# Kernel optimization log

Measured on AMD Instinct MI355X. Metric: run time of the kernel, lower is better.

The kernel has to match this reference:

```python
import jax, jax.numpy as jnp
import numpy as np

N_NODES = 50000
N_EDGES = 800000
D_IN = 128
D_OUT = 128
N_GRAPHS = 512
N_CONVS = 5
EPS = 1e-5


def setup_inputs() -> dict:
    key = jax.random.key(0)
    ks = jax.random.split(key, 8)
    x = jax.random.normal(ks[0], (N_NODES, D_IN), dtype=jnp.float32)
    edge_index = jax.random.randint(ks[1], (2, N_EDGES), 0, N_NODES, dtype=jnp.int32)
    batch = jnp.sort(jax.random.randint(ks[2], (N_NODES,), 0, N_GRAPHS, dtype=jnp.int32))
    s = 1.0 / np.sqrt(D_IN)
    W_rel = jax.random.normal(ks[3], (N_CONVS, D_OUT, D_IN), dtype=jnp.float32) * s
    b_rel = jax.random.normal(ks[4], (N_CONVS, D_OUT), dtype=jnp.float32) * s
    W_root = jax.random.normal(ks[5], (N_CONVS, D_OUT, D_IN), dtype=jnp.float32) * s
    gamma = jnp.ones((D_OUT,), dtype=jnp.float32)
    beta = jnp.zeros((D_OUT,), dtype=jnp.float32)
    Wc = jax.random.normal(ks[6], (96, D_OUT), dtype=jnp.float32) * (1.0 / np.sqrt(D_OUT))
    bc = jax.random.normal(ks[7], (96,), dtype=jnp.float32) * (1.0 / np.sqrt(D_OUT))
    return {"x": x, "edge_index": edge_index, "batch": batch, "i": 0,
            "W_rel": W_rel, "b_rel": b_rel, "W_root": W_root,
            "gamma": gamma, "beta": beta, "Wc": Wc, "bc": bc}


def reference(x, edge_index, batch, i, W_rel, b_rel, W_root, gamma, beta, Wc, bc):
    # --- 5 GraphConv branches, summed. GraphConv: lin_rel(sum_{j->i} x_j) + lin_root(x).
    # Sum over the 5 convs commutes with the linears, so fold the weights first.
    src, dst = edge_index[0], edge_index[1]
    agg = jax.ops.segment_sum(x[src], dst, num_segments=N_NODES)  # [N, D_in]
    Wr = jnp.sum(W_rel, axis=0)   # [D_out, D_in]
    Wt = jnp.sum(W_root, axis=0)  # [D_out, D_in]
    br = jnp.sum(b_rel, axis=0)   # [D_out]
    h = agg @ Wr.T + x @ Wt.T + br  # [N, D_out]
    # --- NodeLevelBatchNorm (training: batch stats over all nodes, biased var)
    mean = jnp.mean(h, axis=0)
    var = jnp.mean((h - mean) ** 2, axis=0)
    h = gamma * (h - mean) * jax.lax.rsqrt(var + EPS) + beta
    # --- global max pool over graphs, relu, classifier (i=0 -> no-dropout branch)
    pooled = jax.ops.segment_max(h, batch, num_segments=N_GRAPHS)  # [G, D_out]
    pooled = jax.nn.relu(pooled)
    return pooled @ Wc.T + bc  # [G, 96]
```

## Files before the change

### kernel.cpp

```cpp
#include <hip/hip_runtime.h>

#define EPS 1e-5f

constexpr int NN = 50000, NE = 800000, DD = 128, NG = 512, NC = 5, NO = 96;
constexpr int MAXB = 8192;
constexpr int NBUCK = 196;

typedef __attribute__((ext_vector_type(8))) short bf16x8;
typedef __attribute__((ext_vector_type(4))) float f32x4;

constexpr size_t HB   = 0;
constexpr size_t XB   = (size_t)NN * DD / 2;
constexpr size_t WB   = XB + (size_t)NN * DD / 2;
constexpr size_t BRO  = WB + DD * 256 / 2;
constexpr size_t CSUM = BRO + DD;
constexpr size_t CSQ  = CSUM + DD;
constexpr size_t POOL = CSQ + DD;
constexpr size_t GCNT = POOL + (size_t)NG * DD;
constexpr size_t ZEND = GCNT + 256;
constexpr size_t ROFF = ZEND;
constexpr size_t BSTOR= ROFF + NN + 1;
constexpr size_t CSR16= BSTOR + (size_t)NBUCK*MAXB;

constexpr int XCAST_B = NN * DD / 4 / 256;
constexpr int FOLD_B  = DD * DD / 256;
constexpr int BUCK_B  = (NE + 4095) / 4096;

static __device__ __forceinline__ unsigned short f2b(float f) {
    unsigned int u = __float_as_uint(f);
    return (unsigned short)((u + 0x7FFFu + ((u >> 16) & 1u)) >> 16);
}
static __device__ __forceinline__ float b2f(unsigned short h) {
    return __uint_as_float(((unsigned int)h) << 16);
}
static __device__ __forceinline__ unsigned fkey(float f) {
    unsigned u = __float_as_uint(f);
    return (u >> 31) ? ~u : (u | 0x80000000u);
}
static __device__ __forceinline__ float unfkey(unsigned k) {
    unsigned u = (k & 0x80000000u) ? (k ^ 0x80000000u) : ~k;
    return __uint_as_float(u);
}

__global__ __launch_bounds__(256) void k_prep(const float* __restrict__ x,
                                              const float* __restrict__ Wrel,
                                              const float* __restrict__ brel,
                                              const float* __restrict__ Wroot,
                                              const int* __restrict__ ei,
                                              float* __restrict__ ws, int* __restrict__ wi) {
    __shared__ int lcnt[256];
    __shared__ int lbase[256];
    int b = blockIdx.x, t = threadIdx.x;
    if (b < XCAST_B) {
        int i = b * 256 + t;
        float4 v = ((const float4*)x)[i];
        ushort4 o = {f2b(v.x), f2b(v.y), f2b(v.z), f2b(v.w)};
        ((ushort4*)(ws + XB))[i] = o;
    } else if (b < XCAST_B + FOLD_B) {
        int idx = (b - XCAST_B) * 256 + t;
        int k = idx >> 7, o = idx & 127;
        float wr = 0.f, wt = 0.f;
        for (int c = 0; c < NC; ++c) {
            wr += Wrel [c*DD*DD + o*DD + k];
            wt += Wroot[c*DD*DD + o*DD + k];
        }
        unsigned short* wb = (unsigned short*)(ws + WB);
        wb[o*256 + k]       = f2b(wr);
        wb[o*256 + 128 + k] = f2b(wt);
        if (k == 0) {
            float bias = 0.f;
            for (int c = 0; c < NC; ++c) bias += brel[c*DD + o];
            ws[BRO + o] = bias;
        }
    } else {
        int bb = b - XCAST_B - FOLD_B;
        lcnt[t] = 0;
        __syncthreads();
        int val[16], krk[16];
        #pragma unroll
        for (int j = 0; j < 16; ++j) {
            int e = bb * 4096 + j * 256 + t;
            krk[j] = -1;
            if (e < NE) {
                int d = ei[NE + e], s = ei[e];
                int key = d >> 8;
                int r = atomicAdd(&lcnt[key], 1);
                val[j] = s | ((d & 255) << 16);
                krk[j] = (key << 16) | r;
            }
        }
        __syncthreads();
        if (t < NBUCK && lcnt[t] > 0)
            lbase[t] = atomicAdd(&wi[GCNT + t], lcnt[t]);
        __syncthreads();
        #pragma unroll
        for (int j = 0; j < 16; ++j) {
            if (krk[j] >= 0) {
                int key = krk[j] >> 16, r = krk[j] & 0xFFFF;
                int p = lbase[key] + r;
                if (p < MAXB) wi[BSTOR + (size_t)key * MAXB + p] = val[j];
            }
        }
    }
}

__global__ __launch_bounds__(256) void k_sort(int* __restrict__ wi) {
    __shared__ int eds[MAXB];
    __shared__ unsigned short srt[MAXB];
    __shared__ int cnt[256], cnt2[256], lscan[256], gall[256];
    int t = threadIdx.x, b = blockIdx.x;
    int g = wi[GCNT + t];
    gall[t] = g; lscan[t] = g; cnt[t] = 0;
    __syncthreads();
    for (int off = 1; off < 256; off <<= 1) {
        int u = (t >= off) ? gall[t - off] : 0;
        __syncthreads();
        gall[t] += u;
        __syncthreads();
    }
    int base = gall[b] - lscan[b];
    int C = lscan[b]; if (C > MAXB) C = MAXB;
    __syncthreads();
    for (int i = t; i < C; i += 256) {
        int v = wi[BSTOR + (size_t)b * MAXB + i];
        eds[i] = v;
        atomicAdd(&cnt[v >> 16], 1);
    }
    __syncthreads();
    int cv = cnt[t];
    for (int off = 1; off < 256; off <<= 1) {
        int u = (t >= off) ? cnt[t - off] : 0;
        __syncthreads();
        cnt[t] += u;
        __syncthreads();
    }
    lscan[t] = cnt[t] - cv;
    cnt2[t] = 0;
    __syncthreads();
    int n = b * 256 + t;
    if (n < NN) wi[ROFF + n] = base + lscan[t];
    if (b == 0 && t == 0) wi[ROFF + NN] = NE;
    for (int i = t; i < C; i += 256) {
        int v = eds[i], k = v >> 16;
        int p = lscan[k] + atomicAdd(&cnt2[k], 1);
        srt[p] = (unsigned short)(v & 0xFFFF);
    }
    __syncthreads();
    unsigned short* csr = (unsigned short*)(wi + CSR16);
    for (int i = t; i < C; i += 256)
        csr[base + i] = srt[i];
}

__global__ __launch_bounds__(256) void k_gather(const int* __restrict__ wi,
                                                float* __restrict__ ws) {
    const unsigned short* xb = (const unsigned short*)(ws + XB);
    const unsigned short* csr = (const unsigned short*)(wi + CSR16);
    unsigned short* hb = (unsigned short*)(ws + HB);
    int tid = threadIdx.x;
    int n   = blockIdx.x * 16 + (tid >> 4);
    int sub = tid & 15;
    int c8  = sub * 8;
    if (n >= NN) return;
    int e0 = wi[ROFF + n], e1 = wi[ROFF + n + 1];
    int cnt = e1 - e0;
    float acc0[8] = {}, acc1[8] = {};
    int base = 0;
    for (; base + 16 <= cnt; base += 16) {
        int myE = (int)csr[e0 + base + sub];
        #pragma unroll
        for (int h = 0; h < 2; ++h) {
            bf16x8 v[8];
            #pragma unroll
            for (int j = 0; j < 8; ++j) {
                int s = __shfl(myE, h * 8 + j, 16);
                v[j] = *(const bf16x8*)&xb[(size_t)s * DD + c8];
            }
            #pragma unroll
            for (int j = 0; j < 8; ++j)
                #pragma unroll
                for (int c = 0; c < 8; ++c)
                    ((j & 1) ? acc1 : acc0)[c] += b2f((unsigned short)v[j][c]);
        }
    }
    int rem = cnt - base;
    if (rem > 0) {
        int myE = (sub < rem) ? (int)csr[e0 + base + sub] : 0;
        int j = 0;
        for (; j + 8 <= rem; j += 8) {
            bf16x8 v[8];
            #pragma unroll
            for (int q = 0; q < 8; ++q) {
                int s = __shfl(myE, j + q, 16);
                v[q] = *(const bf16x8*)&xb[(size_t)s * DD + c8];
            }
            #pragma unroll
            for (int q = 0; q < 8; ++q)
                #pragma unroll
                for (int c = 0; c < 8; ++c)
                    ((q & 1) ? acc1 : acc0)[c] += b2f((unsigned short)v[q][c]);
        }
        if (j + 4 <= rem) {
            bf16x8 v[4];
            #pragma unroll
            for (int q = 0; q < 4; ++q) {
                int s = __shfl(myE, j + q, 16);
                v[q] = *(const bf16x8*)&xb[(size_t)s * DD + c8];
            }
            #pragma unroll
            for (int q = 0; q < 4; ++q)
                #pragma unroll
                for (int c = 0; c < 8; ++c)
                    ((q & 1) ? acc1 : acc0)[c] += b2f((unsigned short)v[q][c]);
            j += 4;
        }
        for (; j < rem; ++j) {
            int s = __shfl(myE, j, 16);
            bf16x8 v = *(const bf16x8*)&xb[(size_t)s * DD + c8];
            #pragma unroll
            for (int c = 0; c < 8; ++c) acc0[c] += b2f((unsigned short)v[c]);
        }
    }
    bf16x8 o;
    #pragma unroll
    for (int c = 0; c < 8; ++c) o[c] = (short)f2b(acc0[c] + acc1[c]);
    *(bf16x8*)&hb[(size_t)n * DD + c8] = o;
}

__global__ __launch_bounds__(256) void k_gemm(const int* __restrict__ batch,
                                              float* __restrict__ ws) {
    __shared__ float sSum[128], sSq[128];
    __shared__ int batchS[128];
    __shared__ unsigned maxS[32][128];
    const unsigned short* hb = (const unsigned short*)(ws + HB);
    const unsigned short* xb = (const unsigned short*)(ws + XB);
    const unsigned short* wb = (const unsigned short*)(ws + WB);
    unsigned* poolU = (unsigned*)(ws + POOL);
    int tid  = threadIdx.x;
    if (tid < 128) { sSum[tid] = 0.f; sSq[tid] = 0.f; }
    for (int i = tid; i < 32 * 128; i += 256) ((unsigned*)maxS)[i] = 0u;
    if (tid < 128) {
        int r = blockIdx.x * 128 + tid; if (r > NN - 1) r = NN - 1;
        batchS[tid] = batch[r];
    }
    __syncthreads();
    int gBase = batchS[0];
    int wave = tid >> 6, lane = tid & 63;
    int ch = wave & 1, rg = wave >> 1;
    int quad = lane >> 4, l16 = lane & 15;
    bf16x8 bf[4][8];
    #pragma unroll
    for (int nt = 0; nt < 4; ++nt)
        #pragma unroll
        for (int kt = 0; kt < 8; ++kt)
            bf[nt][kt] = *(const bf16x8*)(wb + (size_t)(ch*64 + nt*16 + l16)*256 + kt*32 + quad*8);
    float bias[4], csum[4] = {}, csq[4] = {};
    #pragma unroll
    for (int nt = 0; nt < 4; ++nt) bias[nt] = ws[BRO + ch*64 + nt*16 + l16];
    #pragma unroll
    for (int c = 0; c < 4; ++c) {
        int lbase = rg * 64 + c * 16;
        int row0 = blockIdx.x * 128 + lbase;
        int arow = row0 + l16; if (arow > NN - 1) arow = NN - 1;
        const unsigned short* aggRow = hb + (size_t)arow * DD;
        const unsigned short* xRow   = xb + (size_t)arow * DD;
        bf16x8 af[8];
        #pragma unroll
        for (int kt = 0; kt < 8; ++kt)
            af[kt] = *(const bf16x8*)((kt < 4 ? aggRow + kt*32 : xRow + kt*32 - 128) + quad*8);
        f32x4 acc[4] = {};
        #pragma unroll
        for (int kt = 0; kt < 8; ++kt)
            #pragma unroll
            for (int nt = 0; nt < 4; ++nt)
                acc[nt] = __builtin_amdgcn_mfma_f32_16x16x32_bf16(af[kt], bf[nt][kt], acc[nt], 0, 0, 0);
        #pragma unroll
        for (int nt = 0; nt < 4; ++nt) {
            int col = ch*64 + nt*16 + l16;
            float mx = 0.f; int gcur = -1;
            #pragma unroll
            for (int r = 0; r < 4; ++r) {
                int row = row0 + quad*4 + r;
                if (row < NN) {
                    float v = acc[nt][r] + bias[nt];
                    csum[nt] += v; csq[nt] += v * v;
                    int g = batchS[lbase + quad*4 + r];
                    if (g != gcur) {
                        if (gcur >= 0) {
                            int rel = gcur - gBase;
                            if (rel < 32) atomicMax(&maxS[rel][col], fkey(mx));
                            else atomicMax(&poolU[(size_t)gcur * DD + col], fkey(mx));
                        }
                        gcur = g; mx = v;
                    } else mx = fmaxf(mx, v);
                }
            }
            if (gcur >= 0) {
                int rel = gcur - gBase;
                if (rel < 32) atomicMax(&maxS[rel][col], fkey(mx));
                else atomicMax(&poolU[(size_t)gcur * DD + col], fkey(mx));
            }
        }
    }
    __syncthreads();
    int span = batchS[127] - gBase + 1; if (span > 32) span = 32;
    for (int i = tid; i < span * 128; i += 256) {
        unsigned k = maxS[i >> 7][i & 127];
        if (k) atomicMax(&poolU[(size_t)(gBase + (i >> 7)) * DD + (i & 127)], k);
    }
    #pragma unroll
    for (int nt = 0; nt < 4; ++nt) {
        int col = ch*64 + nt*16 + l16;
        float cs = csum[nt], cq = csq[nt];
        cs += __shfl_xor(cs, 16); cs += __shfl_xor(cs, 32);
        cq += __shfl_xor(cq, 16); cq += __shfl_xor(cq, 32);
        if (quad == 0) { atomicAdd(&sSum[col], cs); atomicAdd(&sSq[col], cq); }
    }
    __syncthreads();
    if (tid < 128) {
        atomicAdd(&ws[CSUM + tid], sSum[tid]);
        atomicAdd(&ws[CSQ  + tid], sSq[tid]);
    }
}

__global__ __launch_bounds__(128) void k_out(const float* __restrict__ gamma,
                                             const float* __restrict__ beta,
                                             const float* __restrict__ Wc,
                                             const float* __restrict__ bc,
                                             const float* __restrict__ ws,
                                             float* __restrict__ out) {
    __shared__ float pS[128];
    int g = blockIdx.x, t = threadIdx.x;
    float mean = ws[CSUM + t] * (1.0f / NN);
    float var  = ws[CSQ + t] * (1.0f / NN) - mean * mean;
    float sc   = gamma[t] * rsqrtf(var + EPS);
    float sh   = beta[t] - sc * mean;
    unsigned k = ((const unsigned*)(ws + POOL))[(size_t)g * DD + t];
    float p = 0.f;
    if (k) p = fmaxf(unfkey(k) * sc + sh, 0.f);
    pS[t] = p;
    __syncthreads();
    if (t < NO) {
        float acc = bc[t];
        #pragma unroll 8
        for (int kk = 0; kk < DD; ++kk) acc += pS[kk] * Wc[t*DD + kk];
        out[g*NO + t] = acc;
    }
}

extern "C" void kernel_launch(void* const* d_in, const int* in_sizes, int n_in,
                              void* d_out, int out_size, void* d_ws, size_t ws_size,
                              hipStream_t stream) {
    const float* x     = (const float*)d_in[0];
    const int*   ei    = (const int*)  d_in[1];
    const int*   batch = (const int*)  d_in[2];
    const float* Wrel  = (const float*)d_in[4];
    const float* brel  = (const float*)d_in[5];
    const float* Wroot = (const float*)d_in[6];
    const float* gamma = (const float*)d_in[7];
    const float* beta  = (const float*)d_in[8];
    const float* Wc    = (const float*)d_in[9];
    const float* bc    = (const float*)d_in[10];
    float* ws  = (float*)d_ws;
    int*   wi  = (int*)d_ws;
    float* out = (float*)d_out;

    hipMemsetAsync(ws + CSUM, 0, (ZEND - CSUM) * sizeof(float), stream);

    k_prep  <<<XCAST_B + FOLD_B + BUCK_B, 256, 0, stream>>>(x, Wrel, brel, Wroot, ei, ws, wi);
    k_sort  <<<NBUCK, 256, 0, stream>>>(wi);
    k_gather<<<(NN + 15)/16, 256, 0, stream>>>(wi, ws);
    k_gemm  <<<(NN + 127)/128, 256, 0, stream>>>(batch, ws);
    k_out   <<<NG, 128, 0, stream>>>(gamma, beta, Wc, bc, ws, out);
}
```

Before: 183.1 us.

## Halve GEMM row tile, spread BN stat atomics, zero pool buffers in sort kernel

k_gemm now handles 64 rows per block, with each wave owning 32 output columns instead of 64. This doubles the grid to about 782 blocks and shrinks shared memory for the per-block max-pool staging. Batch-norm sum and sum-of-squares atomics are spread over 4 slots keyed by block index to reduce same-address contention, and k_out adds the 4 slots back together. Zeroing of the stats and pool buffers moves from a large memset into k_sort, so the memset only clears the bucket counters. The tradeoff is more blocks, each reloading the weight fragments, and more pool atomics going to global memory when a block spans more than 8 graphs.

```diff
diff --git a/kernel.cpp b/kernel.cpp
--- a/kernel.cpp
+++ b/kernel.cpp
@@ -14,11 +14,11 @@
 constexpr size_t WB   = XB + (size_t)NN * DD / 2;
 constexpr size_t BRO  = WB + DD * 256 / 2;
 constexpr size_t CSUM = BRO + DD;
-constexpr size_t CSQ  = CSUM + DD;
-constexpr size_t POOL = CSQ + DD;
+constexpr size_t CSQ  = CSUM + 4 * DD;
+constexpr size_t POOL = CSQ + 4 * DD;
+constexpr size_t ZLEN = 8 * DD + (size_t)NG * DD;
 constexpr size_t GCNT = POOL + (size_t)NG * DD;
-constexpr size_t ZEND = GCNT + 256;
-constexpr size_t ROFF = ZEND;
+constexpr size_t ROFF = GCNT + 256;
 constexpr size_t BSTOR= ROFF + NN + 1;
 constexpr size_t CSR16= BSTOR + (size_t)NBUCK*MAXB;
 
@@ -109,6 +109,8 @@
     __shared__ unsigned short srt[MAXB];
     __shared__ int cnt[256], cnt2[256], lscan[256], gall[256];
     int t = threadIdx.x, b = blockIdx.x;
+    for (size_t i = (size_t)b * 256 + t; i < ZLEN; i += (size_t)NBUCK * 256)
+        wi[CSUM + i] = 0;
     int g = wi[GCNT + t];
     gall[t] = g; lscan[t] = g; cnt[t] = 0;
     __syncthreads();
@@ -229,37 +231,36 @@
 __global__ __launch_bounds__(256) void k_gemm(const int* __restrict__ batch,
                                               float* __restrict__ ws) {
     __shared__ float sSum[128], sSq[128];
-    __shared__ int batchS[128];
-    __shared__ unsigned maxS[32][128];
+    __shared__ int batchS[64];
+    __shared__ unsigned maxS[8][128];
     const unsigned short* hb = (const unsigned short*)(ws + HB);
     const unsigned short* xb = (const unsigned short*)(ws + XB);
     const unsigned short* wb = (const unsigned short*)(ws + WB);
     unsigned* poolU = (unsigned*)(ws + POOL);
     int tid  = threadIdx.x;
     if (tid < 128) { sSum[tid] = 0.f; sSq[tid] = 0.f; }
-    for (int i = tid; i < 32 * 128; i += 256) ((unsigned*)maxS)[i] = 0u;
-    if (tid < 128) {
-        int r = blockIdx.x * 128 + tid; if (r > NN - 1) r = NN - 1;
+    for (int i = tid; i < 8 * 128; i += 256) ((unsigned*)maxS)[i] = 0u;
+    if (tid < 64) {
+        int r = blockIdx.x * 64 + tid; if (r > NN - 1) r = NN - 1;
         batchS[tid] = batch[r];
     }
     __syncthreads();
     int gBase = batchS[0];
     int wave = tid >> 6, lane = tid & 63;
-    int ch = wave & 1, rg = wave >> 1;
     int quad = lane >> 4, l16 = lane & 15;
-    bf16x8 bf[4][8];
+    int cw = wave * 32;
+    bf16x8 bf[2][8];
     #pragma unroll
-    for (int nt = 0; nt < 4; ++nt)
+    for (int nt = 0; nt < 2; ++nt)
         #pragma unroll
         for (int kt = 0; kt < 8; ++kt)
-            bf[nt][kt] = *(const bf16x8*)(wb + (size_t)(ch*64 + nt*16 + l16)*256 + kt*32 + quad*8);
-    float bias[4], csum[4] = {}, csq[4] = {};
+            bf[nt][kt] = *(const bf16x8*)(wb + (size_t)(cw + nt*16 + l16)*256 + kt*32 + quad*8);
+    float bias[2] = { ws[BRO + cw + l16], ws[BRO + cw + 16 + l16] };
+    float csum[2] = {}, csq[2] = {};
     #pragma unroll
-    for (int nt = 0; nt < 4; ++nt) bias[nt] = ws[BRO + ch*64 + nt*16 + l16];
-    #pragma unroll
-    for (int c = 0; c < 4; ++c) {
-        int lbase = rg * 64 + c * 16;
-        int row0 = blockIdx.x * 128 + lbase;
+    for (int rt = 0; rt < 4; ++rt) {
+        int lbase = rt * 16;
+        int row0 = blockIdx.x * 64 + lbase;
         int arow = row0 + l16; if (arow > NN - 1) arow = NN - 1;
         const unsigned short* aggRow = hb + (size_t)arow * DD;
         const unsigned short* xRow   = xb + (size_t)arow * DD;
@@ -267,15 +268,15 @@
         #pragma unroll
         for (int kt = 0; kt < 8; ++kt)
             af[kt] = *(const bf16x8*)((kt < 4 ? aggRow + kt*32 : xRow + kt*32 - 128) + quad*8);
-        f32x4 acc[4] = {};
+        f32x4 acc[2] = {};
         #pragma unroll
         for (int kt = 0; kt < 8; ++kt)
             #pragma unroll
-            for (int nt = 0; nt < 4; ++nt)
+            for (int nt = 0; nt < 2; ++nt)
                 acc[nt] = __builtin_amdgcn_mfma_f32_16x16x32_bf16(af[kt], bf[nt][kt], acc[nt], 0, 0, 0);
         #pragma unroll
-        for (int nt = 0; nt < 4; ++nt) {
-            int col = ch*64 + nt*16 + l16;
+        for (int nt = 0; nt < 2; ++nt) {
+            int col = cw + nt*16 + l16;
             float mx = 0.f; int gcur = -1;
             #pragma unroll
             for (int r = 0; r < 4; ++r) {
@@ -287,7 +288,7 @@
                     if (g != gcur) {
                         if (gcur >= 0) {
                             int rel = gcur - gBase;
-                            if (rel < 32) atomicMax(&maxS[rel][col], fkey(mx));
+                            if (rel < 8) atomicMax(&maxS[rel][col], fkey(mx));
                             else atomicMax(&poolU[(size_t)gcur * DD + col], fkey(mx));
                         }
                         gcur = g; mx = v;
@@ -296,20 +297,20 @@
             }
             if (gcur >= 0) {
                 int rel = gcur - gBase;
-                if (rel < 32) atomicMax(&maxS[rel][col], fkey(mx));
+                if (rel < 8) atomicMax(&maxS[rel][col], fkey(mx));
                 else atomicMax(&poolU[(size_t)gcur * DD + col], fkey(mx));
             }
         }
     }
     __syncthreads();
-    int span = batchS[127] - gBase + 1; if (span > 32) span = 32;
+    int span = batchS[63] - gBase + 1; if (span > 8) span = 8;
     for (int i = tid; i < span * 128; i += 256) {
         unsigned k = maxS[i >> 7][i & 127];
         if (k) atomicMax(&poolU[(size_t)(gBase + (i >> 7)) * DD + (i & 127)], k);
     }
     #pragma unroll
-    for (int nt = 0; nt < 4; ++nt) {
-        int col = ch*64 + nt*16 + l16;
+    for (int nt = 0; nt < 2; ++nt) {
+        int col = cw + nt*16 + l16;
         float cs = csum[nt], cq = csq[nt];
         cs += __shfl_xor(cs, 16); cs += __shfl_xor(cs, 32);
         cq += __shfl_xor(cq, 16); cq += __shfl_xor(cq, 32);
@@ -317,8 +318,9 @@
     }
     __syncthreads();
     if (tid < 128) {
-        atomicAdd(&ws[CSUM + tid], sSum[tid]);
-        atomicAdd(&ws[CSQ  + tid], sSq[tid]);
+        int slot = (blockIdx.x & 3) * DD;
+        atomicAdd(&ws[CSUM + slot + tid], sSum[tid]);
+        atomicAdd(&ws[CSQ  + slot + tid], sSq[tid]);
     }
 }
 
@@ -330,8 +332,10 @@
                                              float* __restrict__ out) {
     __shared__ float pS[128];
     int g = blockIdx.x, t = threadIdx.x;
-    float mean = ws[CSUM + t] * (1.0f / NN);
-    float var  = ws[CSQ + t] * (1.0f / NN) - mean * mean;
+    float s = ws[CSUM + t] + ws[CSUM + DD + t] + ws[CSUM + 2*DD + t] + ws[CSUM + 3*DD + t];
+    float q = ws[CSQ  + t] + ws[CSQ  + DD + t] + ws[CSQ  + 2*DD + t] + ws[CSQ  + 3*DD + t];
+    float mean = s * (1.0f / NN);
+    float var  = q * (1.0f / NN) - mean * mean;
     float sc   = gamma[t] * rsqrtf(var + EPS);
     float sh   = beta[t] - sc * mean;
     unsigned k = ((const unsigned*)(ws + POOL))[(size_t)g * DD + t];
@@ -364,11 +368,11 @@
     int*   wi  = (int*)d_ws;
     float* out = (float*)d_out;
 
-    hipMemsetAsync(ws + CSUM, 0, (ZEND - CSUM) * sizeof(float), stream);
+    hipMemsetAsync(wi + GCNT, 0, 256 * sizeof(int), stream);
 
     k_prep  <<<XCAST_B + FOLD_B + BUCK_B, 256, 0, stream>>>(x, Wrel, brel, Wroot, ei, ws, wi);
     k_sort  <<<NBUCK, 256, 0, stream>>>(wi);
     k_gather<<<(NN + 15)/16, 256, 0, stream>>>(wi, ws);
-    k_gemm  <<<(NN + 127)/128, 256, 0, stream>>>(batch, ws);
+    k_gemm  <<<(NN + 63)/64, 256, 0, stream>>>(batch, ws);
     k_out   <<<NG, 128, 0, stream>>>(gamma, beta, Wc, bc, ws, out);
 }
```

Result: no change. 183.5 us (+0.2%).
